# Kernel optimization log

Hardware: AMD Instinct MI355X
Metric: run time of the kernel (lower is better)

The kernel has to match this reference:

```python
import jax, jax.numpy as jnp
import numpy as np

B, N, D, K = 16, 65536, 24, 512
ATTRACTION_WEIGHT = 1.0
REPULSION_WEIGHT = 1.5
MARGIN_WEIGHT = 5.0
THRESHOLD = 0.5
MARGIN = 0.2
TAU = 0.7


def setup_inputs() -> dict:
    key = jax.random.key(0)
    k1, k2, k3 = jax.random.split(key, 3)
    beta = jax.random.normal(k1, (B, N, 1), jnp.float32)
    embed = jax.random.normal(k2, (B, N, D), jnp.float32)
    # First K hits of each event are the condensation points (one per instance),
    # remaining hits get a random instance id in [0, K).
    rand_sid = jax.random.randint(k3, (B, N - K), 0, K, jnp.int32)
    cp_sid = jnp.broadcast_to(jnp.arange(K, dtype=jnp.int32), (B, K))
    slice_id = jnp.concatenate([cp_sid, rand_sid], axis=1)
    is_cp = jnp.concatenate(
        [jnp.ones((B, K), jnp.int32), jnp.zeros((B, N - K), jnp.int32)], axis=1)
    return {"beta": beta, "embed": embed, "slice_id": slice_id, "is_cp": is_cp}


def _per_batch(beta_b, emb_b, sid, cp):
    # beta_b: [N], emb_b: [N, D], sid: [N] int, cp: [N] int
    n = beta_b.shape[0]
    f32 = beta_b.dtype
    cp_mask = cp == 1
    pos_count = cp_mask.sum()
    neg_count = n - pos_count

    seg_cnt = jax.ops.segment_sum(jnp.ones((n,), f32), sid, num_segments=K)
    inst_present = seg_cnt > 0
    cp_per_inst = jax.ops.segment_sum(cp_mask.astype(f32), sid, num_segments=K)
    valid_inst = inst_present & (cp_per_inst == 1)  # inst_cp.sum() == 1

    # --- grouped softmax CE over each instance (temperature TAU) ---
    logits = jnp.clip(beta_b, -20.0, 20.0) / TAU
    seg_max = jax.ops.segment_max(logits, sid, num_segments=K)
    safe_max = jnp.where(inst_present, seg_max, 0.0)
    ex = jnp.exp(logits - safe_max[sid])
    denom = jax.ops.segment_sum(ex, sid, num_segments=K)
    cp_logit = jax.ops.segment_sum(jnp.where(cp_mask, logits, 0.0), sid,
                                   num_segments=K)  # exactly one cp when valid
    p_cp = jnp.exp(cp_logit - safe_max) / jnp.maximum(denom, 1e-30)
    loss_inst = -jnp.log(p_cp + 1e-9)
    slice_count = valid_inst.sum()
    beta_slice_ce = jnp.where(valid_inst, loss_inst, 0.0).sum() / jnp.maximum(slice_count, 1)

    # --- margin loss on sigmoid(beta) ---
    beta_prob = jax.nn.sigmoid(jnp.clip(beta_b, -20.0, 20.0))
    pos_m = jnp.where(cp_mask, jax.nn.relu(THRESHOLD + MARGIN - beta_prob), 0.0).sum() \
        / jnp.maximum(pos_count, 1)
    neg_m = jnp.where(cp_mask, 0.0, jax.nn.relu(beta_prob - (THRESHOLD - MARGIN))).sum() \
        / jnp.maximum(neg_count, 1)
    beta_loss = beta_slice_ce + MARGIN_WEIGHT * (pos_m + neg_m)

    # --- attraction: hits pulled to first CP of their instance ---
    idx = jnp.arange(n, dtype=jnp.int32)
    first_cp = jax.ops.segment_min(jnp.where(cp_mask, idx, n), sid, num_segments=K)
    has_cp = (first_cp < n) & inst_present
    cp_emb = emb_b[jnp.minimum(first_cp, n - 1)]  # [K, D]
    d2 = jnp.minimum(((emb_b - cp_emb[sid]) ** 2).sum(-1), 50.0)
    d2_mean = jax.ops.segment_sum(d2, sid, num_segments=K) / jnp.maximum(seg_cnt, 1.0)
    attraction = ATTRACTION_WEIGHT * jnp.where(has_cp, d2_mean, 0.0).sum()

    # --- repulsion: pairwise exp(-d2) between CP embeddings (incl. diagonal) ---
    m = has_cp.astype(f32)
    mcount = m.sum()
    sq = (cp_emb ** 2).sum(-1)
    pd2 = sq[:, None] + sq[None, :] - 2.0 * (cp_emb @ cp_emb.T)
    pd2 = jnp.clip(pd2, 0.0, 50.0)
    rep = (jnp.exp(-pd2) * (m[:, None] * m[None, :])).sum() / jnp.maximum(mcount * mcount, 1.0)
    repulsion = jnp.where(mcount > 1, REPULSION_WEIGHT * rep, 0.0)

    valid = (pos_count >= 1) & (neg_count >= 1) & (slice_count > 0)
    total = beta_loss + attraction + repulsion
    return total, beta_loss, attraction, repulsion, valid


def reference(beta, embed, slice_id, is_cp):
    beta = jnp.nan_to_num(jnp.squeeze(beta, -1), nan=0.0, posinf=0.0, neginf=0.0)
    embed = jnp.nan_to_num(embed, nan=0.0, posinf=0.0, neginf=0.0)
    total, bl, al, rl, valid = jax.vmap(_per_batch)(beta, embed, slice_id, is_cp)
    v = valid.astype(beta.dtype)
    count = v.sum()
    safe = jnp.maximum(count, 1.0)
    ok = count > 0
    final = jnp.where(ok, (total * v).sum() / safe, 0.0)
    beta_log = jnp.where(ok, (bl * v).sum() / safe, 0.0)
    attr_log = jnp.where(ok, (al * v).sum() / safe, 0.0)
    repl_log = jnp.where(ok, (rl * v).sum() / safe, 0.0)
    return final, beta_log, attr_log, repl_log
```

## Files before the change

### kernel.cpp

```cpp
#include <hip/hip_runtime.h>
#include <math.h>

#define BB 16
#define NN 65536
#define DD 24
#define KK 512
#define CH 64
#define HPB (NN / CH)
#define TPB 256
#define RPB 8

__device__ __forceinline__ float fixnum(float v) {
  return __builtin_isfinite(v) ? v : 0.0f;
}

__device__ __forceinline__ float blockReduceSum(float v, float* sbuf) {
  __syncthreads();
  #pragma unroll
  for (int off = 32; off > 0; off >>= 1) v += __shfl_down(v, off, 64);
  int wid = threadIdx.x >> 6, lane = threadIdx.x & 63;
  if (lane == 0) sbuf[wid] = v;
  __syncthreads();
  return sbuf[0] + sbuf[1] + sbuf[2] + sbuf[3];
}

__global__ __launch_bounds__(TPB) void k1_seg(
    const float* __restrict__ beta, const int* __restrict__ sid,
    const int* __restrict__ iscp,
    float* __restrict__ cnt_p, float* __restrict__ den_p,
    float* __restrict__ cpc_p, float* __restrict__ cpl_p,
    int* __restrict__ first_p, float* __restrict__ marg_p)
{
  __shared__ float s_cnt[KK], s_den[KK], s_cpc[KK], s_cpl[KK];
  __shared__ int   s_first[KK];
  __shared__ float sred[4];
  int b = blockIdx.x >> 6, c = blockIdx.x & 63, t = threadIdx.x;
  for (int k = t; k < KK; k += TPB) {
    s_cnt[k] = 0.f; s_den[k] = 0.f; s_cpc[k] = 0.f; s_cpl[k] = 0.f; s_first[k] = NN;
  }
  __syncthreads();
  int h0 = c * HPB + t * 4;
  size_t g0 = (size_t)b * NN + h0;
  float4 bv = *(const float4*)(beta + g0);
  int4   sv = *(const int4*)(sid + g0);
  int4   cv = *(const int4*)(iscp + g0);
  float pm = 0.f, nm = 0.f;
  float bs[4] = {bv.x, bv.y, bv.z, bv.w};
  int   ss[4] = {sv.x, sv.y, sv.z, sv.w};
  int   cs[4] = {cv.x, cv.y, cv.z, cv.w};
  #pragma unroll
  for (int j = 0; j < 4; ++j) {
    float bc = fminf(fmaxf(fixnum(bs[j]), -20.f), 20.f);
    float logit = bc * (1.0f / 0.7f);
    int s = ss[j];
    atomicAdd(&s_cnt[s], 1.0f);
    atomicAdd(&s_den[s], __expf(logit));
    float prob = 1.0f / (1.0f + __expf(-bc));
    if (cs[j] == 1) {
      atomicAdd(&s_cpc[s], 1.0f);
      atomicAdd(&s_cpl[s], logit);
      atomicMin(&s_first[s], h0 + j);
      pm += fmaxf(0.7f - prob, 0.f);
    } else {
      nm += fmaxf(prob - 0.3f, 0.f);
    }
  }
  float pms = blockReduceSum(pm, sred);
  float nms = blockReduceSum(nm, sred);
  if (t == 0) { marg_p[2 * blockIdx.x] = pms; marg_p[2 * blockIdx.x + 1] = nms; }
  __syncthreads();
  size_t base = ((size_t)b * CH + c) * KK;
  for (int k = t; k < KK; k += TPB) {
    cnt_p[base + k] = s_cnt[k]; den_p[base + k] = s_den[k];
    cpc_p[base + k] = s_cpc[k]; cpl_p[base + k] = s_cpl[k];
    first_p[base + k] = s_first[k];
  }
}

__global__ __launch_bounds__(TPB) void k2_fin(
    const float* __restrict__ embed,
    const float* __restrict__ cnt_p, const float* __restrict__ den_p,
    const float* __restrict__ cpc_p, const float* __restrict__ cpl_p,
    const int* __restrict__ first_p,
    float* __restrict__ seg_cnt, float* __restrict__ loss_v,
    float* __restrict__ valid_f, float* __restrict__ has_cp_f,
    float* __restrict__ cpc_tot, float* __restrict__ cp_emb,
    float* __restrict__ d2_acc, float* __restrict__ rep_acc)
{
  int idx = blockIdx.x * TPB + threadIdx.x;
  int b = idx >> 9, k = idx & (KK - 1);
  float cnt = 0.f, den = 0.f, cpc = 0.f, cpl = 0.f;
  int fc = NN;
  #pragma unroll 8
  for (int c = 0; c < CH; ++c) {
    size_t base = ((size_t)b * CH + c) * KK + k;
    cnt += cnt_p[base]; den += den_p[base];
    cpc += cpc_p[base]; cpl += cpl_p[base];
    fc = min(fc, first_p[base]);
  }
  bool present = cnt > 0.f;
  bool vinst = present && (cpc == 1.0f);
  float p = __expf(cpl) / fmaxf(den, 1e-30f);
  seg_cnt[idx] = cnt;
  cpc_tot[idx] = cpc;
  loss_v[idx] = vinst ? -__logf(p + 1e-9f) : 0.f;
  valid_f[idx] = vinst ? 1.f : 0.f;
  has_cp_f[idx] = ((fc < NN) && present) ? 1.f : 0.f;
  d2_acc[idx] = 0.f;
  if (idx < BB) rep_acc[idx] = 0.f;
  int row = fc < NN ? fc : NN - 1;
  const float4* src = (const float4*)(embed + ((size_t)b * NN + row) * DD);
  float4* dst = (float4*)(cp_emb + (size_t)idx * DD);
  #pragma unroll
  for (int q = 0; q < DD / 4; ++q) {
    float4 v = src[q];
    v.x = fixnum(v.x); v.y = fixnum(v.y); v.z = fixnum(v.z); v.w = fixnum(v.w);
    dst[q] = v;
  }
}

__global__ __launch_bounds__(TPB) void k3_attr_rep(
    const float* __restrict__ embed, const int* __restrict__ sid,
    const float* __restrict__ cp_emb, const float* __restrict__ has_cp_f,
    float* __restrict__ d2_acc, float* __restrict__ rep_acc)
{
  __shared__ float s_d2[KK];
  __shared__ float sred[4];
  int b = blockIdx.x >> 6, c = blockIdx.x & 63, t = threadIdx.x;
  for (int k = t; k < KK; k += TPB) s_d2[k] = 0.f;
  __syncthreads();
  const float* cebase = cp_emb + (size_t)b * KK * DD;
  #pragma unroll
  for (int i = 0; i < HPB / TPB; ++i) {
    int h = c * HPB + i * TPB + t;
    size_t g = (size_t)b * NN + h;
    int s = sid[g];
    const float4* e  = (const float4*)(embed + g * DD);
    const float4* ce = (const float4*)(cebase + (size_t)s * DD);
    float d2 = 0.f;
    #pragma unroll
    for (int q = 0; q < DD / 4; ++q) {
      float4 ev = e[q]; float4 cv = ce[q];
      float x;
      x = fixnum(ev.x) - cv.x; d2 += x * x;
      x = fixnum(ev.y) - cv.y; d2 += x * x;
      x = fixnum(ev.z) - cv.z; d2 += x * x;
      x = fixnum(ev.w) - cv.w; d2 += x * x;
    }
    atomicAdd(&s_d2[s], fminf(d2, 50.f));
  }
  __syncthreads();
  for (int k = t; k < KK; k += TPB)
    atomicAdd(&d2_acc[b * KK + k], s_d2[k]);

  int j0 = t, j1 = t + TPB;
  float cj0[DD], cj1[DD];
  const float4* cj0p = (const float4*)(cebase + (size_t)j0 * DD);
  const float4* cj1p = (const float4*)(cebase + (size_t)j1 * DD);
  #pragma unroll
  for (int q = 0; q < DD / 4; ++q) {
    float4 a = cj0p[q], bq = cj1p[q];
    cj0[q*4] = a.x; cj0[q*4+1] = a.y; cj0[q*4+2] = a.z; cj0[q*4+3] = a.w;
    cj1[q*4] = bq.x; cj1[q*4+1] = bq.y; cj1[q*4+2] = bq.z; cj1[q*4+3] = bq.w;
  }
  float m0 = has_cp_f[b * KK + j0], m1 = has_cp_f[b * KK + j1];
  float acc = 0.f;
  #pragma unroll
  for (int ri = 0; ri < RPB; ++ri) {
    int i = c * RPB + ri;
    float mi = has_cp_f[b * KK + i];
    float d20 = 0.f, d21 = 0.f;
    #pragma unroll
    for (int d = 0; d < DD; ++d) {
      float ci = cebase[i * DD + d];
      float x0 = ci - cj0[d]; d20 += x0 * x0;
      float x1 = ci - cj1[d]; d21 += x1 * x1;
    }
    acc += mi * (m0 * __expf(-fminf(d20, 50.f)) + m1 * __expf(-fminf(d21, 50.f)));
  }
  float tot = blockReduceSum(acc, sred);
  if (t == 0) atomicAdd(&rep_acc[b], tot);
}

__global__ __launch_bounds__(1024) void k4_final(
    const float* __restrict__ d2_acc, const float* __restrict__ seg_cnt,
    const float* __restrict__ loss_v, const float* __restrict__ valid_f,
    const float* __restrict__ cpc_tot, const float* __restrict__ has_cp_f,
    const float* __restrict__ marg_p, const float* __restrict__ rep_acc,
    float* __restrict__ out)
{
  __shared__ float s_b[BB][5];
  int w = threadIdx.x >> 6, l = threadIdx.x & 63;
  int b = w;
  float attr = 0.f, ce = 0.f, vcnt = 0.f, pcnt = 0.f, mcnt = 0.f;
  #pragma unroll
  for (int k = l; k < KK; k += 64) {
    int idx = b * KK + k;
    float hc = has_cp_f[idx];
    attr += hc * (d2_acc[idx] / fmaxf(seg_cnt[idx], 1.f));
    ce   += loss_v[idx];
    vcnt += valid_f[idx];
    pcnt += cpc_tot[idx];
    mcnt += hc;
  }
  float pm = marg_p[(b * CH + l) * 2];
  float nm = marg_p[(b * CH + l) * 2 + 1];
  #pragma unroll
  for (int off = 32; off > 0; off >>= 1) {
    attr += __shfl_down(attr, off, 64);
    ce   += __shfl_down(ce, off, 64);
    vcnt += __shfl_down(vcnt, off, 64);
    pcnt += __shfl_down(pcnt, off, 64);
    mcnt += __shfl_down(mcnt, off, 64);
    pm   += __shfl_down(pm, off, 64);
    nm   += __shfl_down(nm, off, 64);
  }
  if (l == 0) {
    float pos = pcnt, neg = (float)NN - pos;
    float slice_ce = ce / fmaxf(vcnt, 1.f);
    float beta_loss = slice_ce + 5.0f * (pm / fmaxf(pos, 1.f) + nm / fmaxf(neg, 1.f));
    float rep = rep_acc[b] / fmaxf(mcnt * mcnt, 1.f);
    float repulsion = (mcnt > 1.f) ? 1.5f * rep : 0.f;
    float v = (pos >= 1.f && neg >= 1.f && vcnt > 0.f) ? 1.f : 0.f;
    s_b[w][0] = (beta_loss + attr + repulsion) * v;
    s_b[w][1] = beta_loss * v;
    s_b[w][2] = attr * v;
    s_b[w][3] = repulsion * v;
    s_b[w][4] = v;
  }
  __syncthreads();
  if (threadIdx.x == 0) {
    float s0 = 0.f, s1 = 0.f, s2 = 0.f, s3 = 0.f, cv = 0.f;
    #pragma unroll
    for (int i = 0; i < BB; ++i) {
      s0 += s_b[i][0]; s1 += s_b[i][1]; s2 += s_b[i][2]; s3 += s_b[i][3]; cv += s_b[i][4];
    }
    float safe = fmaxf(cv, 1.f);
    bool ok = cv > 0.f;
    out[0] = ok ? s0 / safe : 0.f;
    out[1] = ok ? s1 / safe : 0.f;
    out[2] = ok ? s2 / safe : 0.f;
    out[3] = ok ? s3 / safe : 0.f;
  }
}

extern "C" void kernel_launch(void* const* d_in, const int* in_sizes, int n_in,
                              void* d_out, int out_size, void* d_ws, size_t ws_size,
                              hipStream_t stream) {
  (void)in_sizes; (void)n_in; (void)out_size; (void)ws_size;
  const float* beta  = (const float*)d_in[0];
  const float* embed = (const float*)d_in[1];
  const int*   sid   = (const int*)d_in[2];
  const int*   iscp  = (const int*)d_in[3];
  float* out = (float*)d_out;
  char* ws = (char*)d_ws;

  size_t off = 0;
  auto alloc = [&](size_t bytes) {
    size_t o = off; off += (bytes + 255) & ~(size_t)255; return o;
  };
  const size_t BCK = (size_t)BB * CH * KK * 4;
  const size_t BKf = (size_t)BB * KK * 4;
  size_t o_cnt_p  = alloc(BCK);
  size_t o_den_p  = alloc(BCK);
  size_t o_cpc_p  = alloc(BCK);
  size_t o_cpl_p  = alloc(BCK);
  size_t o_first  = alloc(BCK);
  size_t o_marg   = alloc((size_t)BB * CH * 2 * 4);
  size_t o_segc   = alloc(BKf);
  size_t o_lossv  = alloc(BKf);
  size_t o_validf = alloc(BKf);
  size_t o_hascp  = alloc(BKf);
  size_t o_cpct   = alloc(BKf);
  size_t o_d2     = alloc(BKf);
  size_t o_cpe    = alloc((size_t)BB * KK * DD * 4);
  size_t o_rep    = alloc((size_t)BB * 4);

  k1_seg<<<BB * CH, TPB, 0, stream>>>(beta, sid, iscp,
      (float*)(ws + o_cnt_p), (float*)(ws + o_den_p),
      (float*)(ws + o_cpc_p), (float*)(ws + o_cpl_p),
      (int*)(ws + o_first), (float*)(ws + o_marg));

  k2_fin<<<(BB * KK) / TPB, TPB, 0, stream>>>(embed,
      (const float*)(ws + o_cnt_p), (const float*)(ws + o_den_p),
      (const float*)(ws + o_cpc_p), (const float*)(ws + o_cpl_p),
      (const int*)(ws + o_first),
      (float*)(ws + o_segc), (float*)(ws + o_lossv), (float*)(ws + o_validf),
      (float*)(ws + o_hascp), (float*)(ws + o_cpct), (float*)(ws + o_cpe),
      (float*)(ws + o_d2), (float*)(ws + o_rep));

  k3_attr_rep<<<BB * CH, TPB, 0, stream>>>(embed, sid,
      (const float*)(ws + o_cpe), (const float*)(ws + o_hascp),
      (float*)(ws + o_d2), (float*)(ws + o_rep));

  k4_final<<<1, 1024, 0, stream>>>((const float*)(ws + o_d2),
      (const float*)(ws + o_segc), (const float*)(ws + o_lossv),
      (const float*)(ws + o_validf), (const float*)(ws + o_cpct),
      (const float*)(ws + o_hascp), (const float*)(ws + o_marg),
      (const float*)(ws + o_rep), out);
}
```

Before: 200.2 us.

## Stage condensation embeddings and coalesced hit tiles in LDS for attraction kernel

The attraction/repulsion kernel now copies each batch's full condensation-point embedding table (48KB) into shared memory and reads it there instead of through gathered global loads. Hit embeddings are loaded as coalesced float2 chunks into a padded LDS tile, with the next tile prefetched into registers. Four threads split each hit's 24 dimensions and combine partial sums with shuffles. This removes uncoalesced per-thread 96-byte strided loads and scattered global gathers. In exchange it uses much more LDS per block, which lowers occupancy, and adds a barrier per tile.

```diff
diff --git a/kernel.cpp b/kernel.cpp
--- a/kernel.cpp
+++ b/kernel.cpp
@@ -124,44 +124,75 @@
     const float* __restrict__ cp_emb, const float* __restrict__ has_cp_f,
     float* __restrict__ d2_acc, float* __restrict__ rep_acc)
 {
+  __shared__ __align__(16) float s_ce[KK * DD];
+  __shared__ float s_tile[64 * 25];
   __shared__ float s_d2[KK];
-  __shared__ float sred[4];
   int b = blockIdx.x >> 6, c = blockIdx.x & 63, t = threadIdx.x;
+
+  const float4* ceg = (const float4*)(cp_emb + (size_t)b * KK * DD);
+  float4* ces = (float4*)s_ce;
+  #pragma unroll
+  for (int i = 0; i < (KK * DD / 4) / TPB; ++i)
+    ces[t + i * TPB] = ceg[t + i * TPB];
   for (int k = t; k < KK; k += TPB) s_d2[k] = 0.f;
-  __syncthreads();
-  const float* cebase = cp_emb + (size_t)b * KK * DD;
-  #pragma unroll
-  for (int i = 0; i < HPB / TPB; ++i) {
-    int h = c * HPB + i * TPB + t;
-    size_t g = (size_t)b * NN + h;
-    int s = sid[g];
-    const float4* e  = (const float4*)(embed + g * DD);
-    const float4* ce = (const float4*)(cebase + (size_t)s * DD);
+
+  int hl = t >> 2, q = t & 3, d0 = q * 6;
+  int rbase = hl * 25 + d0;
+  int wI[3];
+  #pragma unroll
+  for (int j = 0; j < 3; ++j) {
+    int f = 2 * (t + j * TPB);
+    int h = f / 24;
+    wI[j] = h * 25 + (f - h * 24);
+  }
+
+  size_t hit0 = (size_t)b * NN + (size_t)c * HPB;
+  const float2* eb2 = (const float2*)(embed + hit0 * DD);
+  const int* sidb = sid + hit0;
+
+  float2 r[3];
+  #pragma unroll
+  for (int j = 0; j < 3; ++j) r[j] = eb2[t + j * TPB];
+  __syncthreads();
+
+  for (int tile = 0; tile < 16; ++tile) {
+    #pragma unroll
+    for (int j = 0; j < 3; ++j) {
+      s_tile[wI[j]]     = fixnum(r[j].x);
+      s_tile[wI[j] + 1] = fixnum(r[j].y);
+    }
+    __syncthreads();
+    if (tile < 15) {
+      const float2* nb = eb2 + (size_t)(tile + 1) * (64 * DD / 2);
+      #pragma unroll
+      for (int j = 0; j < 3; ++j) r[j] = nb[t + j * TPB];
+    }
+    int s = sidb[tile * 64 + hl];
+    int cbase = s * DD + d0;
     float d2 = 0.f;
     #pragma unroll
-    for (int q = 0; q < DD / 4; ++q) {
-      float4 ev = e[q]; float4 cv = ce[q];
-      float x;
-      x = fixnum(ev.x) - cv.x; d2 += x * x;
-      x = fixnum(ev.y) - cv.y; d2 += x * x;
-      x = fixnum(ev.z) - cv.z; d2 += x * x;
-      x = fixnum(ev.w) - cv.w; d2 += x * x;
-    }
-    atomicAdd(&s_d2[s], fminf(d2, 50.f));
-  }
-  __syncthreads();
+    for (int d = 0; d < 6; ++d) {
+      float x = s_tile[rbase + d] - s_ce[cbase + d];
+      d2 += x * x;
+    }
+    d2 += __shfl_xor(d2, 1, 64);
+    d2 += __shfl_xor(d2, 2, 64);
+    if (q == 0) atomicAdd(&s_d2[s], fminf(d2, 50.f));
+    __syncthreads();
+  }
+
   for (int k = t; k < KK; k += TPB)
     atomicAdd(&d2_acc[b * KK + k], s_d2[k]);
 
   int j0 = t, j1 = t + TPB;
   float cj0[DD], cj1[DD];
-  const float4* cj0p = (const float4*)(cebase + (size_t)j0 * DD);
-  const float4* cj1p = (const float4*)(cebase + (size_t)j1 * DD);
-  #pragma unroll
-  for (int q = 0; q < DD / 4; ++q) {
-    float4 a = cj0p[q], bq = cj1p[q];
-    cj0[q*4] = a.x; cj0[q*4+1] = a.y; cj0[q*4+2] = a.z; cj0[q*4+3] = a.w;
-    cj1[q*4] = bq.x; cj1[q*4+1] = bq.y; cj1[q*4+2] = bq.z; cj1[q*4+3] = bq.w;
+  const float4* cj0p = (const float4*)(s_ce + j0 * DD);
+  const float4* cj1p = (const float4*)(s_ce + j1 * DD);
+  #pragma unroll
+  for (int qq = 0; qq < DD / 4; ++qq) {
+    float4 a = cj0p[qq], bq = cj1p[qq];
+    cj0[qq*4] = a.x; cj0[qq*4+1] = a.y; cj0[qq*4+2] = a.z; cj0[qq*4+3] = a.w;
+    cj1[qq*4] = bq.x; cj1[qq*4+1] = bq.y; cj1[qq*4+2] = bq.z; cj1[qq*4+3] = bq.w;
   }
   float m0 = has_cp_f[b * KK + j0], m1 = has_cp_f[b * KK + j1];
   float acc = 0.f;
@@ -172,13 +203,13 @@
     float d20 = 0.f, d21 = 0.f;
     #pragma unroll
     for (int d = 0; d < DD; ++d) {
-      float ci = cebase[i * DD + d];
+      float ci = s_ce[i * DD + d];
       float x0 = ci - cj0[d]; d20 += x0 * x0;
       float x1 = ci - cj1[d]; d21 += x1 * x1;
     }
     acc += mi * (m0 * __expf(-fminf(d20, 50.f)) + m1 * __expf(-fminf(d21, 50.f)));
   }
-  float tot = blockReduceSum(acc, sred);
+  float tot = blockReduceSum(acc, s_d2);
   if (t == 0) atomicAdd(&rep_acc[b], tot);
 }
 
```

Result: slower. 206.1 us (+2.9%).

## Stage cp embeddings in LDS, split k2 reduction, fuse final via ticket

Applied to the files above, without the earlier changes.

k2 now uses four threads per (batch, instance) pair, each summing a quarter of the chunk partials before a shuffle combine, which gives more parallelism over the partial-sum reads. k3 copies the 48 KB block of condensation-point embeddings for its batch into shared memory and reads both the attraction gathers and the repulsion rows from there instead of global memory. The final reduction kernel is removed: the last block to finish k3, found with an atomic ticket, does the per-batch reduction and writes the output, saving one launch. In exchange, the larger LDS use (about 55 KB per block) may lower occupancy, and correctness now depends on the fence-and-ticket ordering.

```diff
diff --git a/kernel.cpp b/kernel.cpp
--- a/kernel.cpp
+++ b/kernel.cpp
@@ -85,58 +85,81 @@
     float* __restrict__ seg_cnt, float* __restrict__ loss_v,
     float* __restrict__ valid_f, float* __restrict__ has_cp_f,
     float* __restrict__ cpc_tot, float* __restrict__ cp_emb,
-    float* __restrict__ d2_acc, float* __restrict__ rep_acc)
+    float* __restrict__ d2_acc, float* __restrict__ rep_acc,
+    int* __restrict__ ticket)
 {
-  int idx = blockIdx.x * TPB + threadIdx.x;
-  int b = idx >> 9, k = idx & (KK - 1);
+  int g = blockIdx.x * TPB + threadIdx.x;
+  int pair = g >> 2, sub = g & 3;
+  int b = pair >> 9, k = pair & (KK - 1);
   float cnt = 0.f, den = 0.f, cpc = 0.f, cpl = 0.f;
   int fc = NN;
-  #pragma unroll 8
-  for (int c = 0; c < CH; ++c) {
+  #pragma unroll
+  for (int j = 0; j < CH / 4; ++j) {
+    int c = sub * (CH / 4) + j;
     size_t base = ((size_t)b * CH + c) * KK + k;
     cnt += cnt_p[base]; den += den_p[base];
     cpc += cpc_p[base]; cpl += cpl_p[base];
     fc = min(fc, first_p[base]);
   }
-  bool present = cnt > 0.f;
-  bool vinst = present && (cpc == 1.0f);
-  float p = __expf(cpl) / fmaxf(den, 1e-30f);
-  seg_cnt[idx] = cnt;
-  cpc_tot[idx] = cpc;
-  loss_v[idx] = vinst ? -__logf(p + 1e-9f) : 0.f;
-  valid_f[idx] = vinst ? 1.f : 0.f;
-  has_cp_f[idx] = ((fc < NN) && present) ? 1.f : 0.f;
-  d2_acc[idx] = 0.f;
-  if (idx < BB) rep_acc[idx] = 0.f;
-  int row = fc < NN ? fc : NN - 1;
-  const float4* src = (const float4*)(embed + ((size_t)b * NN + row) * DD);
-  float4* dst = (float4*)(cp_emb + (size_t)idx * DD);
-  #pragma unroll
-  for (int q = 0; q < DD / 4; ++q) {
-    float4 v = src[q];
-    v.x = fixnum(v.x); v.y = fixnum(v.y); v.z = fixnum(v.z); v.w = fixnum(v.w);
-    dst[q] = v;
-  }
+  cnt += __shfl_xor(cnt, 1, 64); cnt += __shfl_xor(cnt, 2, 64);
+  den += __shfl_xor(den, 1, 64); den += __shfl_xor(den, 2, 64);
+  cpc += __shfl_xor(cpc, 1, 64); cpc += __shfl_xor(cpc, 2, 64);
+  cpl += __shfl_xor(cpl, 1, 64); cpl += __shfl_xor(cpl, 2, 64);
+  fc = min(fc, __shfl_xor(fc, 1, 64)); fc = min(fc, __shfl_xor(fc, 2, 64));
+  if (sub == 0) {
+    bool present = cnt > 0.f;
+    bool vinst = present && (cpc == 1.0f);
+    float p = __expf(cpl) / fmaxf(den, 1e-30f);
+    seg_cnt[pair] = cnt;
+    cpc_tot[pair] = cpc;
+    loss_v[pair] = vinst ? -__logf(p + 1e-9f) : 0.f;
+    valid_f[pair] = vinst ? 1.f : 0.f;
+    has_cp_f[pair] = ((fc < NN) && present) ? 1.f : 0.f;
+    d2_acc[pair] = 0.f;
+    if (pair < BB) rep_acc[pair] = 0.f;
+    int row = fc < NN ? fc : NN - 1;
+    const float4* src = (const float4*)(embed + ((size_t)b * NN + row) * DD);
+    float4* dst = (float4*)(cp_emb + (size_t)pair * DD);
+    #pragma unroll
+    for (int q = 0; q < DD / 4; ++q) {
+      float4 v = src[q];
+      v.x = fixnum(v.x); v.y = fixnum(v.y); v.z = fixnum(v.z); v.w = fixnum(v.w);
+      dst[q] = v;
+    }
+  }
+  if (g == 0) *ticket = 0;
 }
 
 __global__ __launch_bounds__(TPB) void k3_attr_rep(
     const float* __restrict__ embed, const int* __restrict__ sid,
     const float* __restrict__ cp_emb, const float* __restrict__ has_cp_f,
-    float* __restrict__ d2_acc, float* __restrict__ rep_acc)
+    float* __restrict__ d2_acc, float* __restrict__ rep_acc,
+    const float* __restrict__ seg_cnt, const float* __restrict__ loss_v,
+    const float* __restrict__ valid_f, const float* __restrict__ cpc_tot,
+    const float* __restrict__ marg_p, int* __restrict__ ticket,
+    float* __restrict__ out)
 {
+  __shared__ float s_ce[KK * DD];
+  __shared__ float s_tile[64 * 25];
   __shared__ float s_d2[KK];
-  __shared__ float sred[4];
+  __shared__ int   s_last;
+  __shared__ float s_fb[BB][5];
   int b = blockIdx.x >> 6, c = blockIdx.x & 63, t = threadIdx.x;
+
+  const float4* ceg = (const float4*)(cp_emb + (size_t)b * KK * DD);
+  float4* ces = (float4*)s_ce;
+  #pragma unroll
+  for (int i = 0; i < (KK * DD / 4) / TPB; ++i)
+    ces[t + i * TPB] = ceg[t + i * TPB];
   for (int k = t; k < KK; k += TPB) s_d2[k] = 0.f;
   __syncthreads();
-  const float* cebase = cp_emb + (size_t)b * KK * DD;
-  #pragma unroll
+
+  int h = c * HPB + t;
   for (int i = 0; i < HPB / TPB; ++i) {
-    int h = c * HPB + i * TPB + t;
-    size_t g = (size_t)b * NN + h;
+    size_t g = (size_t)b * NN + h + i * TPB;
     int s = sid[g];
     const float4* e  = (const float4*)(embed + g * DD);
-    const float4* ce = (const float4*)(cebase + (size_t)s * DD);
+    const float4* ce = (const float4*)(s_ce + (size_t)s * DD);
     float d2 = 0.f;
     #pragma unroll
     for (int q = 0; q < DD / 4; ++q) {
@@ -155,13 +178,13 @@
 
   int j0 = t, j1 = t + TPB;
   float cj0[DD], cj1[DD];
-  const float4* cj0p = (const float4*)(cebase + (size_t)j0 * DD);
-  const float4* cj1p = (const float4*)(cebase + (size_t)j1 * DD);
-  #pragma unroll
-  for (int q = 0; q < DD / 4; ++q) {
-    float4 a = cj0p[q], bq = cj1p[q];
-    cj0[q*4] = a.x; cj0[q*4+1] = a.y; cj0[q*4+2] = a.z; cj0[q*4+3] = a.w;
-    cj1[q*4] = bq.x; cj1[q*4+1] = bq.y; cj1[q*4+2] = bq.z; cj1[q*4+3] = bq.w;
+  const float4* cj0p = (const float4*)(s_ce + j0 * DD);
+  const float4* cj1p = (const float4*)(s_ce + j1 * DD);
+  #pragma unroll
+  for (int qq = 0; qq < DD / 4; ++qq) {
+    float4 a = cj0p[qq], bq = cj1p[qq];
+    cj0[qq*4] = a.x; cj0[qq*4+1] = a.y; cj0[qq*4+2] = a.z; cj0[qq*4+3] = a.w;
+    cj1[qq*4] = bq.x; cj1[qq*4+1] = bq.y; cj1[qq*4+2] = bq.z; cj1[qq*4+3] = bq.w;
   }
   float m0 = has_cp_f[b * KK + j0], m1 = has_cp_f[b * KK + j1];
   float acc = 0.f;
@@ -172,68 +195,67 @@
     float d20 = 0.f, d21 = 0.f;
     #pragma unroll
     for (int d = 0; d < DD; ++d) {
-      float ci = cebase[i * DD + d];
+      float ci = s_ce[i * DD + d];
       float x0 = ci - cj0[d]; d20 += x0 * x0;
       float x1 = ci - cj1[d]; d21 += x1 * x1;
     }
     acc += mi * (m0 * __expf(-fminf(d20, 50.f)) + m1 * __expf(-fminf(d21, 50.f)));
   }
-  float tot = blockReduceSum(acc, sred);
+  float tot = blockReduceSum(acc, s_d2);
   if (t == 0) atomicAdd(&rep_acc[b], tot);
-}
-
-__global__ __launch_bounds__(1024) void k4_final(
-    const float* __restrict__ d2_acc, const float* __restrict__ seg_cnt,
-    const float* __restrict__ loss_v, const float* __restrict__ valid_f,
-    const float* __restrict__ cpc_tot, const float* __restrict__ has_cp_f,
-    const float* __restrict__ marg_p, const float* __restrict__ rep_acc,
-    float* __restrict__ out)
-{
-  __shared__ float s_b[BB][5];
-  int w = threadIdx.x >> 6, l = threadIdx.x & 63;
-  int b = w;
-  float attr = 0.f, ce = 0.f, vcnt = 0.f, pcnt = 0.f, mcnt = 0.f;
-  #pragma unroll
-  for (int k = l; k < KK; k += 64) {
-    int idx = b * KK + k;
-    float hc = has_cp_f[idx];
-    attr += hc * (d2_acc[idx] / fmaxf(seg_cnt[idx], 1.f));
-    ce   += loss_v[idx];
-    vcnt += valid_f[idx];
-    pcnt += cpc_tot[idx];
-    mcnt += hc;
-  }
-  float pm = marg_p[(b * CH + l) * 2];
-  float nm = marg_p[(b * CH + l) * 2 + 1];
-  #pragma unroll
-  for (int off = 32; off > 0; off >>= 1) {
-    attr += __shfl_down(attr, off, 64);
-    ce   += __shfl_down(ce, off, 64);
-    vcnt += __shfl_down(vcnt, off, 64);
-    pcnt += __shfl_down(pcnt, off, 64);
-    mcnt += __shfl_down(mcnt, off, 64);
-    pm   += __shfl_down(pm, off, 64);
-    nm   += __shfl_down(nm, off, 64);
-  }
-  if (l == 0) {
-    float pos = pcnt, neg = (float)NN - pos;
-    float slice_ce = ce / fmaxf(vcnt, 1.f);
-    float beta_loss = slice_ce + 5.0f * (pm / fmaxf(pos, 1.f) + nm / fmaxf(neg, 1.f));
-    float rep = rep_acc[b] / fmaxf(mcnt * mcnt, 1.f);
-    float repulsion = (mcnt > 1.f) ? 1.5f * rep : 0.f;
-    float v = (pos >= 1.f && neg >= 1.f && vcnt > 0.f) ? 1.f : 0.f;
-    s_b[w][0] = (beta_loss + attr + repulsion) * v;
-    s_b[w][1] = beta_loss * v;
-    s_b[w][2] = attr * v;
-    s_b[w][3] = repulsion * v;
-    s_b[w][4] = v;
-  }
-  __syncthreads();
-  if (threadIdx.x == 0) {
+
+  __threadfence();
+  if (t == 0) s_last = (atomicAdd(ticket, 1) == (BB * CH - 1)) ? 1 : 0;
+  __syncthreads();
+  if (s_last == 0) return;
+  __threadfence();
+
+  int w = t >> 6, l = t & 63;
+  for (int bb = w; bb < BB; bb += 4) {
+    float attr = 0.f, ce = 0.f, vcnt = 0.f, pcnt = 0.f, mcnt = 0.f;
+    #pragma unroll
+    for (int k = l; k < KK; k += 64) {
+      int idx = bb * KK + k;
+      float hc = has_cp_f[idx];
+      attr += hc * (d2_acc[idx] / fmaxf(seg_cnt[idx], 1.f));
+      ce   += loss_v[idx];
+      vcnt += valid_f[idx];
+      pcnt += cpc_tot[idx];
+      mcnt += hc;
+    }
+    float pm = marg_p[(bb * CH + l) * 2];
+    float nm = marg_p[(bb * CH + l) * 2 + 1];
+    #pragma unroll
+    for (int off = 32; off > 0; off >>= 1) {
+      attr += __shfl_down(attr, off, 64);
+      ce   += __shfl_down(ce, off, 64);
+      vcnt += __shfl_down(vcnt, off, 64);
+      pcnt += __shfl_down(pcnt, off, 64);
+      mcnt += __shfl_down(mcnt, off, 64);
+      pm   += __shfl_down(pm, off, 64);
+      nm   += __shfl_down(nm, off, 64);
+    }
+    if (l == 0) {
+      float pos = pcnt, neg = (float)NN - pos;
+      float slice_ce = ce / fmaxf(vcnt, 1.f);
+      float beta_loss = slice_ce + 5.0f * (pm / fmaxf(pos, 1.f) + nm / fmaxf(neg, 1.f));
+      float rep = rep_acc[bb] / fmaxf(mcnt * mcnt, 1.f);
+      float repulsion = (mcnt > 1.f) ? 1.5f * rep : 0.f;
+      float v = (pos >= 1.f && neg >= 1.f && vcnt > 0.f) ? 1.f : 0.f;
+      s_fb[bb][0] = (beta_loss + attr + repulsion) * v;
+      s_fb[bb][1] = beta_loss * v;
+      s_fb[bb][2] = attr * v;
+      s_fb[bb][3] = repulsion * v;
+      s_fb[bb][4] = v;
+    }
+  }
+  __syncthreads();
+  if (t == 0) {
     float s0 = 0.f, s1 = 0.f, s2 = 0.f, s3 = 0.f, cv = 0.f;
     #pragma unroll
     for (int i = 0; i < BB; ++i) {
-      s0 += s_b[i][0]; s1 += s_b[i][1]; s2 += s_b[i][2]; s3 += s_b[i][3]; cv += s_b[i][4];
+      s0 += s_fb[i][0]; s1 += s_fb[i][1]; s2 += s_fb[i][2]; s3 += s_fb[i][3];
+      cv += s_fb[i][4];
     }
     float safe = fmaxf(cv, 1.f);
     bool ok = cv > 0.f;
@@ -275,27 +297,32 @@
   size_t o_d2     = alloc(BKf);
   size_t o_cpe    = alloc((size_t)BB * KK * DD * 4);
   size_t o_rep    = alloc((size_t)BB * 4);
+  size_t o_tick   = alloc(256);
+
+  float* p_cnt  = (float*)(ws + o_cnt_p);
+  float* p_den  = (float*)(ws + o_den_p);
+  float* p_cpc  = (float*)(ws + o_cpc_p);
+  float* p_cpl  = (float*)(ws + o_cpl_p);
+  int*   p_fst  = (int*)(ws + o_first);
+  float* p_marg = (float*)(ws + o_marg);
+  float* p_segc = (float*)(ws + o_segc);
+  float* p_lossv= (float*)(ws + o_lossv);
+  float* p_vldf = (float*)(ws + o_validf);
+  float* p_hcp  = (float*)(ws + o_hascp);
+  float* p_cpct = (float*)(ws + o_cpct);
+  float* p_d2   = (float*)(ws + o_d2);
+  float* p_cpe  = (float*)(ws + o_cpe);
+  float* p_rep  = (float*)(ws + o_rep);
+  int*   p_tick = (int*)(ws + o_tick);
 
   k1_seg<<<BB * CH, TPB, 0, stream>>>(beta, sid, iscp,
-      (float*)(ws + o_cnt_p), (float*)(ws + o_den_p),
-      (float*)(ws + o_cpc_p), (float*)(ws + o_cpl_p),
-      (int*)(ws + o_first), (float*)(ws + o_marg));
-
-  k2_fin<<<(BB * KK) / TPB, TPB, 0, stream>>>(embed,
-      (const float*)(ws + o_cnt_p), (const float*)(ws + o_den_p),
-      (const float*)(ws + o_cpc_p), (const float*)(ws + o_cpl_p),
-      (const int*)(ws + o_first),
-      (float*)(ws + o_segc), (float*)(ws + o_lossv), (float*)(ws + o_validf),
-      (float*)(ws + o_hascp), (float*)(ws + o_cpct), (float*)(ws + o_cpe),
-      (float*)(ws + o_d2), (float*)(ws + o_rep));
+      p_cnt, p_den, p_cpc, p_cpl, p_fst, p_marg);
+
+  k2_fin<<<(4 * BB * KK) / TPB, TPB, 0, stream>>>(embed,
+      p_cnt, p_den, p_cpc, p_cpl, p_fst,
+      p_segc, p_lossv, p_vldf, p_hcp, p_cpct, p_cpe, p_d2, p_rep, p_tick);
 
   k3_attr_rep<<<BB * CH, TPB, 0, stream>>>(embed, sid,
-      (const float*)(ws + o_cpe), (const float*)(ws + o_hascp),
-      (float*)(ws + o_d2), (float*)(ws + o_rep));
-
-  k4_final<<<1, 1024, 0, stream>>>((const float*)(ws + o_d2),
-      (const float*)(ws + o_segc), (const float*)(ws + o_lossv),
-      (const float*)(ws + o_validf), (const float*)(ws + o_cpct),
-      (const float*)(ws + o_hascp), (const float*)(ws + o_marg),
-      (const float*)(ws + o_rep), out);
-}
+      p_cpe, p_hcp, p_d2, p_rep,
+      p_segc, p_lossv, p_vldf, p_cpct, p_marg, p_tick, out);
+}
```

After: 326.1 us. +62.9%, slower.

## Stage condensation-point embeddings in LDS and split k2 chunk reduction across lanes

Applied to the files above, without the earlier changes.

k3 now copies each event's full condensation-point embedding table (512x24 floats, 48KB) into shared memory once per block. The gather and the pairwise repulsion loops then read from LDS instead of scattered global or L2 loads. k2 is split so four lanes each reduce a quarter of the 64 chunk partials and combine them with xor shuffles, which gives 4x more threads for that latency-bound reduction. The trade-off is 48KB of LDS per block in k3, which limits occupancy, plus an extra 48KB copy per block.

```diff
diff --git a/kernel.cpp b/kernel.cpp
--- a/kernel.cpp
+++ b/kernel.cpp
@@ -87,35 +87,44 @@
     float* __restrict__ cpc_tot, float* __restrict__ cp_emb,
     float* __restrict__ d2_acc, float* __restrict__ rep_acc)
 {
-  int idx = blockIdx.x * TPB + threadIdx.x;
-  int b = idx >> 9, k = idx & (KK - 1);
+  int g = blockIdx.x * TPB + threadIdx.x;
+  int pair = g >> 2, sub = g & 3;
+  int b = pair >> 9, k = pair & (KK - 1);
   float cnt = 0.f, den = 0.f, cpc = 0.f, cpl = 0.f;
   int fc = NN;
-  #pragma unroll 8
-  for (int c = 0; c < CH; ++c) {
+  #pragma unroll
+  for (int j = 0; j < CH / 4; ++j) {
+    int c = sub * (CH / 4) + j;
     size_t base = ((size_t)b * CH + c) * KK + k;
     cnt += cnt_p[base]; den += den_p[base];
     cpc += cpc_p[base]; cpl += cpl_p[base];
     fc = min(fc, first_p[base]);
   }
-  bool present = cnt > 0.f;
-  bool vinst = present && (cpc == 1.0f);
-  float p = __expf(cpl) / fmaxf(den, 1e-30f);
-  seg_cnt[idx] = cnt;
-  cpc_tot[idx] = cpc;
-  loss_v[idx] = vinst ? -__logf(p + 1e-9f) : 0.f;
-  valid_f[idx] = vinst ? 1.f : 0.f;
-  has_cp_f[idx] = ((fc < NN) && present) ? 1.f : 0.f;
-  d2_acc[idx] = 0.f;
-  if (idx < BB) rep_acc[idx] = 0.f;
-  int row = fc < NN ? fc : NN - 1;
-  const float4* src = (const float4*)(embed + ((size_t)b * NN + row) * DD);
-  float4* dst = (float4*)(cp_emb + (size_t)idx * DD);
-  #pragma unroll
-  for (int q = 0; q < DD / 4; ++q) {
-    float4 v = src[q];
-    v.x = fixnum(v.x); v.y = fixnum(v.y); v.z = fixnum(v.z); v.w = fixnum(v.w);
-    dst[q] = v;
+  cnt += __shfl_xor(cnt, 1, 64); cnt += __shfl_xor(cnt, 2, 64);
+  den += __shfl_xor(den, 1, 64); den += __shfl_xor(den, 2, 64);
+  cpc += __shfl_xor(cpc, 1, 64); cpc += __shfl_xor(cpc, 2, 64);
+  cpl += __shfl_xor(cpl, 1, 64); cpl += __shfl_xor(cpl, 2, 64);
+  fc = min(fc, __shfl_xor(fc, 1, 64)); fc = min(fc, __shfl_xor(fc, 2, 64));
+  if (sub == 0) {
+    bool present = cnt > 0.f;
+    bool vinst = present && (cpc == 1.0f);
+    float p = __expf(cpl) / fmaxf(den, 1e-30f);
+    seg_cnt[pair] = cnt;
+    cpc_tot[pair] = cpc;
+    loss_v[pair] = vinst ? -__logf(p + 1e-9f) : 0.f;
+    valid_f[pair] = vinst ? 1.f : 0.f;
+    has_cp_f[pair] = ((fc < NN) && present) ? 1.f : 0.f;
+    d2_acc[pair] = 0.f;
+    if (pair < BB) rep_acc[pair] = 0.f;
+    int row = fc < NN ? fc : NN - 1;
+    const float4* src = (const float4*)(embed + ((size_t)b * NN + row) * DD);
+    float4* dst = (float4*)(cp_emb + (size_t)pair * DD);
+    #pragma unroll
+    for (int q = 0; q < DD / 4; ++q) {
+      float4 v = src[q];
+      v.x = fixnum(v.x); v.y = fixnum(v.y); v.z = fixnum(v.z); v.w = fixnum(v.w);
+      dst[q] = v;
+    }
   }
 }
 
@@ -124,19 +133,26 @@
     const float* __restrict__ cp_emb, const float* __restrict__ has_cp_f,
     float* __restrict__ d2_acc, float* __restrict__ rep_acc)
 {
+  __shared__ float s_ce[KK * DD];
   __shared__ float s_d2[KK];
   __shared__ float sred[4];
   int b = blockIdx.x >> 6, c = blockIdx.x & 63, t = threadIdx.x;
+
+  const float4* ceg = (const float4*)(cp_emb + (size_t)b * KK * DD);
+  float4* ces = (float4*)s_ce;
+  #pragma unroll
+  for (int i = 0; i < (KK * DD / 4) / TPB; ++i)
+    ces[t + i * TPB] = ceg[t + i * TPB];
   for (int k = t; k < KK; k += TPB) s_d2[k] = 0.f;
   __syncthreads();
-  const float* cebase = cp_emb + (size_t)b * KK * DD;
+
   #pragma unroll
   for (int i = 0; i < HPB / TPB; ++i) {
     int h = c * HPB + i * TPB + t;
     size_t g = (size_t)b * NN + h;
     int s = sid[g];
     const float4* e  = (const float4*)(embed + g * DD);
-    const float4* ce = (const float4*)(cebase + (size_t)s * DD);
+    const float4* ce = (const float4*)(s_ce + (size_t)s * DD);
     float d2 = 0.f;
     #pragma unroll
     for (int q = 0; q < DD / 4; ++q) {
@@ -155,13 +171,13 @@
 
   int j0 = t, j1 = t + TPB;
   float cj0[DD], cj1[DD];
-  const float4* cj0p = (const float4*)(cebase + (size_t)j0 * DD);
-  const float4* cj1p = (const float4*)(cebase + (size_t)j1 * DD);
-  #pragma unroll
-  for (int q = 0; q < DD / 4; ++q) {
-    float4 a = cj0p[q], bq = cj1p[q];
-    cj0[q*4] = a.x; cj0[q*4+1] = a.y; cj0[q*4+2] = a.z; cj0[q*4+3] = a.w;
-    cj1[q*4] = bq.x; cj1[q*4+1] = bq.y; cj1[q*4+2] = bq.z; cj1[q*4+3] = bq.w;
+  const float4* cj0p = (const float4*)(s_ce + j0 * DD);
+  const float4* cj1p = (const float4*)(s_ce + j1 * DD);
+  #pragma unroll
+  for (int qq = 0; qq < DD / 4; ++qq) {
+    float4 a = cj0p[qq], bq = cj1p[qq];
+    cj0[qq*4] = a.x; cj0[qq*4+1] = a.y; cj0[qq*4+2] = a.z; cj0[qq*4+3] = a.w;
+    cj1[qq*4] = bq.x; cj1[qq*4+1] = bq.y; cj1[qq*4+2] = bq.z; cj1[qq*4+3] = bq.w;
   }
   float m0 = has_cp_f[b * KK + j0], m1 = has_cp_f[b * KK + j1];
   float acc = 0.f;
@@ -172,7 +188,7 @@
     float d20 = 0.f, d21 = 0.f;
     #pragma unroll
     for (int d = 0; d < DD; ++d) {
-      float ci = cebase[i * DD + d];
+      float ci = s_ce[i * DD + d];
       float x0 = ci - cj0[d]; d20 += x0 * x0;
       float x1 = ci - cj1[d]; d21 += x1 * x1;
     }
@@ -281,7 +297,7 @@
       (float*)(ws + o_cpc_p), (float*)(ws + o_cpl_p),
       (int*)(ws + o_first), (float*)(ws + o_marg));
 
-  k2_fin<<<(BB * KK) / TPB, TPB, 0, stream>>>(embed,
+  k2_fin<<<(4 * BB * KK) / TPB, TPB, 0, stream>>>(embed,
       (const float*)(ws + o_cnt_p), (const float*)(ws + o_den_p),
       (const float*)(ws + o_cpc_p), (const float*)(ws + o_cpl_p),
       (const int*)(ws + o_first),
```

Measured after the change: 204.6 us. +2.2%, slower.
